# Kernel optimization log

Measured on AMD Instinct MI355X. Metric: run time of the kernel, lower is better.

Reference implementation:

```python
import jax, jax.numpy as jnp
import numpy as np
import math

B, QL, KL, H, QD, KD, VD = 4, 1024, 1024, 16, 1024, 1024, 1024
QH = QD // H  # 64
KH = KD // H  # 64


def setup_inputs() -> dict:
    rng = jax.random.key(0)
    ks = jax.random.split(rng, 8)
    return {
        "query": jax.random.normal(ks[0], (B, QL, QD), jnp.float32),
        "key": jax.random.normal(ks[1], (B, KL, KD), jnp.float32),
        "value": jax.random.normal(ks[2], (B, KL, VD), jnp.float32),
        "pad_mask": jax.random.randint(ks[3], (B, QL), 0, 2),
        "q_w": jax.random.uniform(ks[4], (H, QL, QH), jnp.float32),
        "k_w": jax.random.uniform(ks[5], (H, KL, KH), jnp.float32),
        "v_w": jax.random.uniform(ks[6], (H, KL, KH), jnp.float32),
        "o_w": jax.random.uniform(ks[7], (H * KH, QD), jnp.float32),
    }


def reference(query, key, value, pad_mask, q_w, k_w, v_w, o_w):
    b = query.shape[0]
    h, ql, qh = q_w.shape
    kl, kh = k_w.shape[1], k_w.shape[2]

    # mask construction: causal (triu, offset 1) OR pad mask tiled as in torch repeat+view
    causal = jnp.triu(jnp.ones((ql, kl), jnp.float32), 1) == 1            # [i, j]
    pad = jnp.tile(pad_mask, (1, kl)).reshape(b, ql, kl) == 1             # [b, i, j]
    mask = causal[None, :, :] | pad                                      # [b, i, j]

    # positional per-head projections: free index of input feature dim is summed out
    wq = jnp.einsum('biq,his->bhis', query, q_w)                          # [b, h, i, s]
    wk = jnp.einsum('bjk,hjt->bhjt', key, k_w)                            # [b, h, j, t]
    wv = jnp.einsum('bjv,hjt->bhjt', value, v_w)                          # [b, h, j, t]

    scale = math.sqrt(h)  # torch uses query.size()[1] == head_num after projection
    scores = jnp.einsum('bhis,bhjs->bhij', wq, wk) / scale                # [b, h, i, j]
    scores = jnp.where(mask[:, None, :, :], -jnp.inf, scores)
    scores = jnp.nan_to_num(scores)  # -inf -> finfo.min, matching torch.nan_to_num

    weight = jax.nn.softmax(scores, axis=0)  # unusual: softmax over the batch axis
    heads = jnp.einsum('bhij,bhjt->bhit', weight, wv)                     # [b, h, i, t]
    heads = heads.reshape(b, -1, h * kh)  # torch .view: reinterprets [h,i,t] as [i, h*t]
    return jnp.einsum('bit,to->bio', heads, o_w)                          # [b, i, q_dim]
```

## Files before the change

### kernel.cpp

```cpp
#include <hip/hip_runtime.h>
#include <hip/hip_bf16.h>

#define NB 4
#define NL 1024
#define NH 16
#define ND 1024
#define HD 64
#define FMIN_F32 (-3.4028234663852886e38f)
#define LOG2E 1.4426950408889634f

typedef __bf16 bf16x8 __attribute__((ext_vector_type(8)));
typedef float f32x4 __attribute__((ext_vector_type(4)));
typedef unsigned int u32;

static __device__ inline unsigned short f2bf(float f) {
    __hip_bfloat16 h = __float2bfloat16(f);
    return __builtin_bit_cast(unsigned short, h);
}

static __device__ inline void bfsplit(float x, unsigned short& hi, unsigned short& lo) {
    unsigned u = __builtin_bit_cast(unsigned, x);
    unsigned r = (u + 0x7FFFu + ((u >> 16) & 1u)) >> 16;
    hi = (unsigned short)r;
    float hf = __builtin_bit_cast(float, r << 16);
    lo = f2bf(x - hf);
}

static __device__ inline u32 pk2(unsigned short a, unsigned short b) {
    return (u32)a | ((u32)b << 16);
}

static __device__ __forceinline__ void gload16(void* lds, const void* g) {
    __builtin_amdgcn_global_load_lds(
        (const __attribute__((address_space(1))) u32*)g,
        (__attribute__((address_space(3))) u32*)lds, 16, 0, 0);
}

__global__ __launch_bounds__(256)
void rowsum_kernel(const float* __restrict__ q, const float* __restrict__ k,
                   const float* __restrict__ v, float* __restrict__ out) {
    int gw   = blockIdx.x * 4 + (threadIdx.x >> 6);
    int lane = threadIdx.x & 63;
    int tensor = gw >> 12;
    int row    = gw & 4095;
    const float* src = tensor == 0 ? q : (tensor == 1 ? k : v);
    const float* p = src + (size_t)row * ND;
    float s = 0.f;
#pragma unroll
    for (int t = 0; t < 4; ++t) {
        float4 x = *reinterpret_cast<const float4*>(p + t * 256 + lane * 4);
        s += (x.x + x.y) + (x.z + x.w);
    }
#pragma unroll
    for (int off = 32; off; off >>= 1) s += __shfl_xor(s, off);
    if (lane == 0) out[tensor * (NB * NL) + row] = s;
}

__global__ __launch_bounds__(256)
void prep_kernel(const float* __restrict__ k_w, const float* __restrict__ v_w,
                 const float* __restrict__ o_w, const float* __restrict__ sums,
                 unsigned short* __restrict__ kPhi, unsigned short* __restrict__ kPlo,
                 unsigned short* __restrict__ vP, unsigned short* __restrict__ BP,
                 float* __restrict__ S) {
    __shared__ float tile[64][132];
    __shared__ float vsL[256];
    const int tid = threadIdx.x;
    const int bx  = blockIdx.x;
    const float* vsum = sums + 2 * NB * NL;
    if (bx < 256) {
        const int h = bx >> 4, jt = bx & 15;
        char* hiT = (char*)kPhi + (size_t)(h * 16 + jt) * 8192;
        char* loT = (char*)kPlo + (size_t)(h * 16 + jt) * 8192;
        const int row = tid >> 2;
        const int s0  = (tid & 3) * 16;
        const float* src = k_w + ((size_t)(h * NL + jt * 64 + row)) * HD + s0;
#pragma unroll
        for (int t = 0; t < 4; ++t) {
            float4 x = reinterpret_cast<const float4*>(src)[t];
            unsigned short h0, h1, h2, h3, l0, l1, l2, l3;
            bfsplit(x.x, h0, l0); bfsplit(x.y, h1, l1);
            bfsplit(x.z, h2, l2); bfsplit(x.w, h3, l3);
            int off = (row * 128 + (s0 + 4 * t) * 2) ^ ((row & 7) << 4);
            *(uint2*)(hiT + off) = make_uint2(pk2(h0, h1), pk2(h2, h3));
            *(uint2*)(loT + off) = make_uint2(pk2(l0, l1), pk2(l2, l3));
        }
    } else if (bx < 512) {
        const int h = (bx - 256) >> 4, jt = (bx - 256) & 15;
#pragma unroll
        for (int t = 0; t < 4; ++t) {
            int id = tid + 256 * t;
            int j = id >> 4, t4 = (id & 15) * 4;
            *(float4*)&tile[j][t4] =
                *(const float4*)(v_w + ((size_t)(h * NL + jt * 64 + j)) * HD + t4);
        }
        vsL[tid] = vsum[(tid >> 6) * NL + jt * 64 + (tid & 63)];
        __syncthreads();
        char* vT_ = (char*)vP + (size_t)(h * 16 + jt) * 8192;
        const int trow = tid >> 2;
        const int jq   = (tid & 3) * 16;
#pragma unroll
        for (int q = 0; q < 4; ++q) {
            int j4 = jq + 4 * q;
            uint2 u;
            u.x = pk2(f2bf(tile[j4 + 0][trow]), f2bf(tile[j4 + 1][trow]));
            u.y = pk2(f2bf(tile[j4 + 2][trow]), f2bf(tile[j4 + 3][trow]));
            int off = (trow * 128 + j4 * 2) ^ ((trow & 7) << 4);
            *(uint2*)(vT_ + off) = u;
        }
        if (jt >= 1) {
            const int b = tid >> 6, t = tid & 63;
            float a = 0.f;
#pragma unroll 16
            for (int j = 0; j < 64; ++j)
                a = fmaf(vsL[b * 64 + j], tile[j][t], a);
            S[(((size_t)h * 16 + jt) * 4 + b) * 64 + t] = a;
        }
    } else {
        const int bxo = bx - 512;
        const int ot = bxo >> 4, kt = bxo & 15;
#pragma unroll
        for (int t = 0; t < 8; ++t) {
            int id = tid + 256 * t;
            int c = id >> 5, o4 = (id & 31) * 4;
            *(float4*)&tile[c][o4] =
                *(const float4*)(o_w + ((size_t)(kt * 64 + c)) * ND + ot * 128 + o4);
        }
        __syncthreads();
        char* bT = (char*)BP + (size_t)(ot * 16 + kt) * 16384;
#pragma unroll
        for (int t = 0; t < 8; ++t) {
            int id = tid + 256 * t;
            int ol = id >> 4, c4 = (id & 15) * 4;
            uint2 u;
            u.x = pk2(f2bf(tile[c4 + 0][ol]), f2bf(tile[c4 + 1][ol]));
            u.y = pk2(f2bf(tile[c4 + 2][ol]), f2bf(tile[c4 + 3][ol]));
            int off = (ol * 128 + c4 * 2) ^ ((ol & 7) << 4);
            *(uint2*)(bT + off) = u;
        }
    }
}

__global__ __launch_bounds__(512, 4)
void attn_kernel(const float* __restrict__ q_w, const int* __restrict__ pad,
                 const float* __restrict__ sums,
                 const unsigned short* __restrict__ kPhi,
                 const unsigned short* __restrict__ kPlo,
                 const unsigned short* __restrict__ vP,
                 const float* __restrict__ S,
                 unsigned short* __restrict__ AP) {
    __shared__ __align__(16) unsigned short kHi[2][4096], kLo[2][4096], vTl[2][4096];
    __shared__ __align__(16) unsigned short qHi[2048], qLo[2048];
    __shared__ __align__(16) unsigned short wlds[8192];
    __shared__ __align__(16) float qs4[128];
    __shared__ __align__(16) float ks4[2][256];
    __shared__ __align__(16) float vs4[2][256];
    __shared__ __align__(16) int   pm4[2][256];

    const float* qsum = sums;
    const float* ksum = sums + NB * NL;
    const float* vsum = sums + 2 * NB * NL;

    const int wid = blockIdx.x;
    const int gq  = wid >> 4;
    const int h   = wid & 15;
    const int itp = (gq < 16) ? (2 * gq) : (63 - 2 * gq);
    const int it0 = itp * 32;
    const int cut = (it0 >> 6) + 1;

    const int tid  = threadIdx.x;
    const int lane = tid & 63;
    const int w    = tid >> 6;
    const int l15  = lane & 15;
    const int kb   = (lane >> 4) * 16;

    {
        int row = tid >> 4;
        int s4  = (tid & 15) * 4;
        float4 x = *(const float4*)(q_w + ((size_t)(h * NL + it0 + row)) * HD + s4);
        unsigned short h0, h1, h2, h3, l0, l1, l2, l3;
        bfsplit(x.x, h0, l0); bfsplit(x.y, h1, l1);
        bfsplit(x.z, h2, l2); bfsplit(x.w, h3, l3);
        int off = (row * 128 + s4 * 2) ^ ((row & 7) << 4);
        *(uint2*)((char*)qHi + off) = make_uint2(pk2(h0, h1), pk2(h2, h3));
        *(uint2*)((char*)qLo + off) = make_uint2(pk2(l0, l1), pk2(l2, l3));
    }
    if (tid < 128) {
        int b = tid >> 5, i = tid & 31;
        qs4[i * 4 + b] = qsum[b * NL + it0 + i];
    }

    auto stage = [&](int buf, int jt) {
        const size_t tb = (size_t)(h * 16 + jt) * 8192 + tid * 16;
        gload16((char*)kHi[buf] + tid * 16, (const char*)kPhi + tb);
        gload16((char*)kLo[buf] + tid * 16, (const char*)kPlo + tb);
        gload16((char*)vTl[buf] + tid * 16, (const char*)vP + tb);
        if (tid < 256) {
            int b = tid >> 6, jj = tid & 63;
            ks4[buf][jj * 4 + b] = ksum[b * NL + jt * 64 + jj] * (LOG2E * 0.25f);
            vs4[buf][jj * 4 + b] = vsum[b * NL + jt * 64 + jj];
            pm4[buf][jj * 4 + b] = pad[b * NL + jt * 64 + jj];
        }
    };

    const int gmi = (w & 1) * 16;
    const int gnj = (w >> 1) * 16;
    const int pb  = w >> 1;
    const int pmh = (w & 1) * 16;

    f32x4 accP[4];
#pragma unroll
    for (int n = 0; n < 4; ++n) accP[n] = (f32x4){0.f, 0.f, 0.f, 0.f};

    stage(0, 0);
    __syncthreads();
    int cur = 0;

    const int i_sm  = gmi + l15;
    const int ig    = it0 + i_sm;
    const int jb_sm = gnj + (lane >> 4) * 4;
    const float4 qsv = *(const float4*)&qs4[i_sm * 4];
    const int woff = (i_sm * 128 + jb_sm * 2) ^ ((i_sm & 7) << 4);

    for (int jt = 0; jt < cut; ++jt) {
        const int j0 = jt * 64;
        if (jt + 1 < cut) stage(cur ^ 1, jt + 1);

        f32x4 gA = (f32x4){0.f, 0.f, 0.f, 0.f};
        f32x4 gB = (f32x4){0.f, 0.f, 0.f, 0.f};
#pragma unroll
        for (int ks = 0; ks < 2; ++ks) {
            const int arow = gnj + l15;
            const int brow = gmi + l15;
            const int aoff = (arow * 128 + ks * 64 + kb) ^ ((arow & 7) << 4);
            const int boff = (brow * 128 + ks * 64 + kb) ^ ((brow & 7) << 4);
            bf16x8 kHiF = __builtin_bit_cast(bf16x8, *(const uint4*)((const char*)kHi[cur] + aoff));
            bf16x8 kLoF = __builtin_bit_cast(bf16x8, *(const uint4*)((const char*)kLo[cur] + aoff));
            bf16x8 qHiF = __builtin_bit_cast(bf16x8, *(const uint4*)((const char*)qHi + boff));
            bf16x8 qLoF = __builtin_bit_cast(bf16x8, *(const uint4*)((const char*)qLo + boff));
            gA = __builtin_amdgcn_mfma_f32_16x16x32_bf16(kHiF, qHiF, gA, 0, 0, 0);
            gA = __builtin_amdgcn_mfma_f32_16x16x32_bf16(kLoF, qHiF, gA, 0, 0, 0);
            gB = __builtin_amdgcn_mfma_f32_16x16x32_bf16(kHiF, qLoF, gB, 0, 0, 0);
        }
        const f32x4 g = gA + gB;

        {
            float wv[4][4];
#pragma unroll
            for (int r = 0; r < 4; ++r) {
                const int j  = jb_sm + r;
                const int jg = j0 + j;
                const float4 ksv = *(const float4*)&ks4[cur][j * 4];
                const float4 vsv = *(const float4*)&vs4[cur][j * 4];
                const int4   pmv = *(const int4*)&pm4[cur][j * 4];
                const float gr = g[r];
                const bool causal = jg > ig;
                const float sb0 = (causal || pmv.x) ? FMIN_F32 : qsv.x * ksv.x * gr;
                const float sb1 = (causal || pmv.y) ? FMIN_F32 : qsv.y * ksv.y * gr;
                const float sb2 = (causal || pmv.z) ? FMIN_F32 : qsv.z * ksv.z * gr;
                const float sb3 = (causal || pmv.w) ? FMIN_F32 : qsv.w * ksv.w * gr;
                const float mx = fmaxf(fmaxf(sb0, sb1), fmaxf(sb2, sb3));
                const float e0 = __builtin_amdgcn_exp2f(sb0 - mx);
                const float e1 = __builtin_amdgcn_exp2f(sb1 - mx);
                const float e2 = __builtin_amdgcn_exp2f(sb2 - mx);
                const float e3 = __builtin_amdgcn_exp2f(sb3 - mx);
                const float inv = __builtin_amdgcn_rcpf((e0 + e1) + (e2 + e3));
                wv[r][0] = e0 * inv * vsv.x;
                wv[r][1] = e1 * inv * vsv.y;
                wv[r][2] = e2 * inv * vsv.z;
                wv[r][3] = e3 * inv * vsv.w;
            }
#pragma unroll
            for (int b = 0; b < 4; ++b) {
                uint2 p;
                p.x = pk2(f2bf(wv[0][b]), f2bf(wv[1][b]));
                p.y = pk2(f2bf(wv[2][b]), f2bf(wv[3][b]));
                *(uint2*)((char*)wlds + b * 4096 + woff) = p;
            }
        }
        asm volatile("s_waitcnt lgkmcnt(0)" ::: "memory");
        __builtin_amdgcn_s_barrier();
        __builtin_amdgcn_sched_barrier(0);

        __builtin_amdgcn_s_setprio(1);
#pragma unroll
        for (int ks = 0; ks < 2; ++ks) {
            const int arow = pmh + l15;
            const int aoff = pb * 4096 + ((arow * 128 + ks * 64 + kb) ^ ((arow & 7) << 4));
            bf16x8 aF = __builtin_bit_cast(bf16x8, *(const uint4*)((const char*)wlds + aoff));
#pragma unroll
            for (int n = 0; n < 4; ++n) {
                const int vrow = n * 16 + l15;
                const int voff = (vrow * 128 + ks * 64 + kb) ^ ((vrow & 7) << 4);
                bf16x8 bF = __builtin_bit_cast(bf16x8, *(const uint4*)((const char*)vTl[cur] + voff));
                accP[n] = __builtin_amdgcn_mfma_f32_16x16x32_bf16(aF, bF, accP[n], 0, 0, 0);
            }
        }
        __builtin_amdgcn_s_setprio(0);
        __syncthreads();
        cur ^= 1;
    }

    if (cut < 16) {
        float sv[4] = {0.f, 0.f, 0.f, 0.f};
        for (int jt = cut; jt < 16; ++jt) {
            const float* sp = S + (((size_t)h * 16 + jt) * 4 + pb) * 64;
#pragma unroll
            for (int n = 0; n < 4; ++n) sv[n] += sp[n * 16 + l15];
        }
#pragma unroll
        for (int n = 0; n < 4; ++n) {
            const float s4v = 0.25f * sv[n];
#pragma unroll
            for (int r = 0; r < 4; ++r) accP[n][r] += s4v;
        }
    }

    {
        const int ib = (it0 + pmh) >> 4;
        char* tbase = (char*)AP + (size_t)((pb * 16 + h) * 16) * 8192;
#pragma unroll
        for (int n = 0; n < 4; ++n)
#pragma unroll
            for (int r = 0; r < 4; ++r) {
                int kt = (lane >> 4) * 4 + r;
                int tt = n * 16 + l15;
                int off = (ib * 128 + tt * 2) ^ ((ib & 7) << 4);
                *(unsigned short*)(tbase + (size_t)kt * 8192 + off) = f2bf(accP[n][r]);
            }
    }
}

__global__ __launch_bounds__(256, 2)
void outgemm_kernel(const unsigned short* __restrict__ AP,
                    const unsigned short* __restrict__ BP,
                    float* __restrict__ out) {
    __shared__ __align__(16) unsigned short aL[3][4096];
    __shared__ __align__(16) unsigned short bL[3][8192];
    const int ox = blockIdx.x;
    const int my = blockIdx.y;
    const int tid  = threadIdx.x;
    const int lane = tid & 63;
    const int w    = tid >> 6;
    const int wr = (w & 1) * 32;
    const int wc = (w >> 1) * 64;
    const int l15  = lane & 15;
    const int kseg = (lane >> 4) * 16;

    f32x4 acc[2][4];
#pragma unroll
    for (int m = 0; m < 2; ++m)
#pragma unroll
        for (int n = 0; n < 4; ++n) acc[m][n] = (f32x4){0.f, 0.f, 0.f, 0.f};

    auto stage = [&](int buf, int kt) {
        const char* at = (const char*)AP + (size_t)(my * 16 + kt) * 8192;
        const char* bt = (const char*)BP + (size_t)(ox * 16 + kt) * 16384;
        gload16((char*)aL[buf] + tid * 16, at + tid * 16);
        gload16((char*)aL[buf] + 4096 + tid * 16, at + 4096 + tid * 16);
#pragma unroll
        for (int r = 0; r < 4; ++r)
            gload16((char*)bL[buf] + r * 4096 + tid * 16, bt + r * 4096 + tid * 16);
    };

    auto compute = [&](int cb) {
        __builtin_amdgcn_s_setprio(1);
#pragma unroll
        for (int ks = 0; ks < 2; ++ks) {
            bf16x8 aF[2], bF[4];
#pragma unroll
            for (int m = 0; m < 2; ++m) {
                int row = wr + m * 16 + l15;
                int off = (row * 128 + ks * 64 + kseg) ^ ((row & 7) << 4);
                aF[m] = __builtin_bit_cast(bf16x8, *(const uint4*)((const char*)aL[cb] + off));
            }
#pragma unroll
            for (int n = 0; n < 4; ++n) {
                int row = wc + n * 16 + l15;
                int off = (row * 128 + ks * 64 + kseg) ^ ((row & 7) << 4);
                bF[n] = __builtin_bit_cast(bf16x8, *(const uint4*)((const char*)bL[cb] + off));
            }
#pragma unroll
            for (int m = 0; m < 2; ++m)
#pragma unroll
                for (int n = 0; n < 4; ++n)
                    acc[m][n] = __builtin_amdgcn_mfma_f32_16x16x32_bf16(
                        aF[m], bF[n], acc[m][n], 0, 0, 0);
        }
        __builtin_amdgcn_s_setprio(0);
    };

    stage(0, 0);
    stage(1, 1);
    for (int kt = 0; kt < 15; ++kt) {
        asm volatile("s_waitcnt vmcnt(6)" ::: "memory");
        __builtin_amdgcn_s_barrier();
        __builtin_amdgcn_sched_barrier(0);
        if (kt + 2 < 16) stage((kt + 2) % 3, kt + 2);
        compute(kt % 3);
    }
    asm volatile("s_waitcnt vmcnt(0)" ::: "memory");
    __builtin_amdgcn_s_barrier();
    __builtin_amdgcn_sched_barrier(0);
    compute(15 % 3);

#pragma unroll
    for (int m = 0; m < 2; ++m)
#pragma unroll
        for (int n = 0; n < 4; ++n)
#pragma unroll
            for (int r = 0; r < 4; ++r) {
                int row = my * 64 + wr + m * 16 + (lane >> 4) * 4 + r;
                int col = ox * 128 + wc + n * 16 + l15;
                out[(size_t)row * ND + col] = acc[m][n][r];
            }
}

extern "C" void kernel_launch(void* const* d_in, const int* in_sizes, int n_in,
                              void* d_out, int out_size, void* d_ws, size_t ws_size,
                              hipStream_t stream) {
    const float* query = (const float*)d_in[0];
    const float* key   = (const float*)d_in[1];
    const float* value = (const float*)d_in[2];
    const int*   pad   = (const int*)d_in[3];
    const float* q_w   = (const float*)d_in[4];
    const float* k_w   = (const float*)d_in[5];
    const float* v_w   = (const float*)d_in[6];
    const float* o_w   = (const float*)d_in[7];
    float* out = (float*)d_out;

    char* W = (char*)d_ws;
    float*          sums = (float*)W;
    unsigned short* kPhi = (unsigned short*)(W + 49152);
    unsigned short* kPlo = (unsigned short*)(W + 2146304);
    unsigned short* vP   = (unsigned short*)(W + 4243456);
    unsigned short* BP   = (unsigned short*)(W + 6340608);
    unsigned short* AP   = (unsigned short*)(W + 8437760);

    float* S = out;

    rowsum_kernel<<<3 * (NB * NL) / 4, 256, 0, stream>>>(query, key, value, sums);

    prep_kernel<<<640, 256, 0, stream>>>(k_w, v_w, o_w, sums, kPhi, kPlo, vP, BP, S);

    attn_kernel<<<512, 512, 0, stream>>>(q_w, pad, sums, kPhi, kPlo, vP, S, AP);

    dim3 gg(8, 64);
    outgemm_kernel<<<gg, 256, 0, stream>>>(AP, BP, out);
}
```

Measured before the change: 69.95 us.

## Precompute masked key/value sums in prep kernel and use packed bf16 conversion

Moves the per-key sum scaling, the pad-mask lookup and the batch interleaving out of the attention kernel's staging loop into extra blocks of the prep kernel. The results are written as interleaved float arrays (scaled key sums, value sums, additive mask bias) into scratch space inside the output buffer, so attention staging becomes three vectorised float4 loads. The score computation turns into an fma plus bias, with a select for the causal case. Scalar bf16 conversion and packing are replaced by the packed v_cvt_pk_bf16_f32 instruction throughout. The trade-off is an extra global round trip for the precomputed arrays and reliance on the output buffer as scratch before the final GEMM overwrites it.

```diff
diff --git a/kernel.cpp b/kernel.cpp
--- a/kernel.cpp
+++ b/kernel.cpp
@@ -18,16 +18,17 @@
     return __builtin_bit_cast(unsigned short, h);
 }
 
-static __device__ inline void bfsplit(float x, unsigned short& hi, unsigned short& lo) {
-    unsigned u = __builtin_bit_cast(unsigned, x);
-    unsigned r = (u + 0x7FFFu + ((u >> 16) & 1u)) >> 16;
-    hi = (unsigned short)r;
-    float hf = __builtin_bit_cast(float, r << 16);
-    lo = f2bf(x - hf);
-}
-
-static __device__ inline u32 pk2(unsigned short a, unsigned short b) {
-    return (u32)a | ((u32)b << 16);
+static __device__ __forceinline__ u32 cvtpk(float a, float b) {
+    u32 r;
+    asm("v_cvt_pk_bf16_f32 %0, %1, %2" : "=v"(r) : "v"(a), "v"(b));
+    return r;
+}
+
+static __device__ __forceinline__ void bfsplit2(float x, float y, u32& hiPk, u32& loPk) {
+    hiPk = cvtpk(x, y);
+    float hx = __builtin_bit_cast(float, hiPk << 16);
+    float hy = __builtin_bit_cast(float, hiPk & 0xffff0000u);
+    loPk = cvtpk(x - hx, y - hy);
 }
 
 static __device__ __forceinline__ void gload16(void* lds, const void* g) {
@@ -59,13 +60,16 @@
 __global__ __launch_bounds__(256)
 void prep_kernel(const float* __restrict__ k_w, const float* __restrict__ v_w,
                  const float* __restrict__ o_w, const float* __restrict__ sums,
+                 const int* __restrict__ pad,
                  unsigned short* __restrict__ kPhi, unsigned short* __restrict__ kPlo,
                  unsigned short* __restrict__ vP, unsigned short* __restrict__ BP,
-                 float* __restrict__ S) {
+                 float* __restrict__ S, float* __restrict__ ksm,
+                 float* __restrict__ vsm, float* __restrict__ bsm) {
     __shared__ float tile[64][132];
     __shared__ float vsL[256];
     const int tid = threadIdx.x;
     const int bx  = blockIdx.x;
+    const float* ksum = sums + NB * NL;
     const float* vsum = sums + 2 * NB * NL;
     if (bx < 256) {
         const int h = bx >> 4, jt = bx & 15;
@@ -77,12 +81,12 @@
 #pragma unroll
         for (int t = 0; t < 4; ++t) {
             float4 x = reinterpret_cast<const float4*>(src)[t];
-            unsigned short h0, h1, h2, h3, l0, l1, l2, l3;
-            bfsplit(x.x, h0, l0); bfsplit(x.y, h1, l1);
-            bfsplit(x.z, h2, l2); bfsplit(x.w, h3, l3);
+            u32 h01, l01, h23, l23;
+            bfsplit2(x.x, x.y, h01, l01);
+            bfsplit2(x.z, x.w, h23, l23);
             int off = (row * 128 + (s0 + 4 * t) * 2) ^ ((row & 7) << 4);
-            *(uint2*)(hiT + off) = make_uint2(pk2(h0, h1), pk2(h2, h3));
-            *(uint2*)(loT + off) = make_uint2(pk2(l0, l1), pk2(l2, l3));
+            *(uint2*)(hiT + off) = make_uint2(h01, h23);
+            *(uint2*)(loT + off) = make_uint2(l01, l23);
         }
     } else if (bx < 512) {
         const int h = (bx - 256) >> 4, jt = (bx - 256) & 15;
@@ -102,8 +106,8 @@
         for (int q = 0; q < 4; ++q) {
             int j4 = jq + 4 * q;
             uint2 u;
-            u.x = pk2(f2bf(tile[j4 + 0][trow]), f2bf(tile[j4 + 1][trow]));
-            u.y = pk2(f2bf(tile[j4 + 2][trow]), f2bf(tile[j4 + 3][trow]));
+            u.x = cvtpk(tile[j4 + 0][trow], tile[j4 + 1][trow]);
+            u.y = cvtpk(tile[j4 + 2][trow], tile[j4 + 3][trow]);
             int off = (trow * 128 + j4 * 2) ^ ((trow & 7) << 4);
             *(uint2*)(vT_ + off) = u;
         }
@@ -115,7 +119,7 @@
                 a = fmaf(vsL[b * 64 + j], tile[j][t], a);
             S[(((size_t)h * 16 + jt) * 4 + b) * 64 + t] = a;
         }
-    } else {
+    } else if (bx < 640) {
         const int bxo = bx - 512;
         const int ot = bxo >> 4, kt = bxo & 15;
 #pragma unroll
@@ -132,21 +136,28 @@
             int id = tid + 256 * t;
             int ol = id >> 4, c4 = (id & 15) * 4;
             uint2 u;
-            u.x = pk2(f2bf(tile[c4 + 0][ol]), f2bf(tile[c4 + 1][ol]));
-            u.y = pk2(f2bf(tile[c4 + 2][ol]), f2bf(tile[c4 + 3][ol]));
+            u.x = cvtpk(tile[c4 + 0][ol], tile[c4 + 1][ol]);
+            u.y = cvtpk(tile[c4 + 2][ol], tile[c4 + 3][ol]);
             int off = (ol * 128 + c4 * 2) ^ ((ol & 7) << 4);
             *(uint2*)(bT + off) = u;
         }
+    } else {
+        const int e = (bx - 640) * 256 + tid;
+        const int j = e >> 2, b = e & 3;
+        const int pm = pad[b * NL + j];
+        ksm[e] = pm ? 0.f : ksum[b * NL + j] * (LOG2E * 0.25f);
+        vsm[e] = vsum[b * NL + j];
+        bsm[e] = pm ? FMIN_F32 : 0.f;
     }
 }
 
 __global__ __launch_bounds__(512, 4)
-void attn_kernel(const float* __restrict__ q_w, const int* __restrict__ pad,
-                 const float* __restrict__ sums,
+void attn_kernel(const float* __restrict__ q_w, const float* __restrict__ sums,
                  const unsigned short* __restrict__ kPhi,
                  const unsigned short* __restrict__ kPlo,
                  const unsigned short* __restrict__ vP,
-                 const float* __restrict__ S,
+                 const float* __restrict__ ksm, const float* __restrict__ vsm,
+                 const float* __restrict__ bsm, const float* __restrict__ S,
                  unsigned short* __restrict__ AP) {
     __shared__ __align__(16) unsigned short kHi[2][4096], kLo[2][4096], vTl[2][4096];
     __shared__ __align__(16) unsigned short qHi[2048], qLo[2048];
@@ -154,11 +165,9 @@
     __shared__ __align__(16) float qs4[128];
     __shared__ __align__(16) float ks4[2][256];
     __shared__ __align__(16) float vs4[2][256];
-    __shared__ __align__(16) int   pm4[2][256];
+    __shared__ __align__(16) float bs4[2][256];
 
     const float* qsum = sums;
-    const float* ksum = sums + NB * NL;
-    const float* vsum = sums + 2 * NB * NL;
 
     const int wid = blockIdx.x;
     const int gq  = wid >> 4;
@@ -177,12 +186,12 @@
         int row = tid >> 4;
         int s4  = (tid & 15) * 4;
         float4 x = *(const float4*)(q_w + ((size_t)(h * NL + it0 + row)) * HD + s4);
-        unsigned short h0, h1, h2, h3, l0, l1, l2, l3;
-        bfsplit(x.x, h0, l0); bfsplit(x.y, h1, l1);
-        bfsplit(x.z, h2, l2); bfsplit(x.w, h3, l3);
+        u32 h01, l01, h23, l23;
+        bfsplit2(x.x, x.y, h01, l01);
+        bfsplit2(x.z, x.w, h23, l23);
         int off = (row * 128 + s4 * 2) ^ ((row & 7) << 4);
-        *(uint2*)((char*)qHi + off) = make_uint2(pk2(h0, h1), pk2(h2, h3));
-        *(uint2*)((char*)qLo + off) = make_uint2(pk2(l0, l1), pk2(l2, l3));
+        *(uint2*)((char*)qHi + off) = make_uint2(h01, h23);
+        *(uint2*)((char*)qLo + off) = make_uint2(l01, l23);
     }
     if (tid < 128) {
         int b = tid >> 5, i = tid & 31;
@@ -190,16 +199,19 @@
     }
 
     auto stage = [&](int buf, int jt) {
+        float4 tv;
+        float* tdst = nullptr;
+        if (tid < 192) {
+            int seg = tid >> 6, l = tid & 63;
+            const float* src = seg == 0 ? ksm : (seg == 1 ? vsm : bsm);
+            tv = *(const float4*)(src + jt * 256 + l * 4);
+            tdst = (seg == 0 ? ks4[buf] : (seg == 1 ? vs4[buf] : bs4[buf])) + l * 4;
+        }
         const size_t tb = (size_t)(h * 16 + jt) * 8192 + tid * 16;
         gload16((char*)kHi[buf] + tid * 16, (const char*)kPhi + tb);
         gload16((char*)kLo[buf] + tid * 16, (const char*)kPlo + tb);
         gload16((char*)vTl[buf] + tid * 16, (const char*)vP + tb);
-        if (tid < 256) {
-            int b = tid >> 6, jj = tid & 63;
-            ks4[buf][jj * 4 + b] = ksum[b * NL + jt * 64 + jj] * (LOG2E * 0.25f);
-            vs4[buf][jj * 4 + b] = vsum[b * NL + jt * 64 + jj];
-            pm4[buf][jj * 4 + b] = pad[b * NL + jt * 64 + jj];
-        }
+        if (tid < 192) *(float4*)tdst = tv;
     };
 
     const int gmi = (w & 1) * 16;
@@ -251,13 +263,17 @@
                 const int jg = j0 + j;
                 const float4 ksv = *(const float4*)&ks4[cur][j * 4];
                 const float4 vsv = *(const float4*)&vs4[cur][j * 4];
-                const int4   pmv = *(const int4*)&pm4[cur][j * 4];
+                const float4 bsv = *(const float4*)&bs4[cur][j * 4];
                 const float gr = g[r];
                 const bool causal = jg > ig;
-                const float sb0 = (causal || pmv.x) ? FMIN_F32 : qsv.x * ksv.x * gr;
-                const float sb1 = (causal || pmv.y) ? FMIN_F32 : qsv.y * ksv.y * gr;
-                const float sb2 = (causal || pmv.z) ? FMIN_F32 : qsv.z * ksv.z * gr;
-                const float sb3 = (causal || pmv.w) ? FMIN_F32 : qsv.w * ksv.w * gr;
+                float sb0 = fmaf(qsv.x * ksv.x, gr, bsv.x);
+                float sb1 = fmaf(qsv.y * ksv.y, gr, bsv.y);
+                float sb2 = fmaf(qsv.z * ksv.z, gr, bsv.z);
+                float sb3 = fmaf(qsv.w * ksv.w, gr, bsv.w);
+                sb0 = causal ? 0.f : sb0;
+                sb1 = causal ? 0.f : sb1;
+                sb2 = causal ? 0.f : sb2;
+                sb3 = causal ? 0.f : sb3;
                 const float mx = fmaxf(fmaxf(sb0, sb1), fmaxf(sb2, sb3));
                 const float e0 = __builtin_amdgcn_exp2f(sb0 - mx);
                 const float e1 = __builtin_amdgcn_exp2f(sb1 - mx);
@@ -272,8 +288,8 @@
 #pragma unroll
             for (int b = 0; b < 4; ++b) {
                 uint2 p;
-                p.x = pk2(f2bf(wv[0][b]), f2bf(wv[1][b]));
-                p.y = pk2(f2bf(wv[2][b]), f2bf(wv[3][b]));
+                p.x = cvtpk(wv[0][b], wv[1][b]);
+                p.y = cvtpk(wv[2][b], wv[3][b]);
                 *(uint2*)((char*)wlds + b * 4096 + woff) = p;
             }
         }
@@ -436,13 +452,18 @@
     unsigned short* BP   = (unsigned short*)(W + 6340608);
     unsigned short* AP   = (unsigned short*)(W + 8437760);
 
-    float* S = out;
+    float* S   = out;
+    float* ksm = out + 65536;
+    float* vsm = out + 69632;
+    float* bsm = out + 73728;
 
     rowsum_kernel<<<3 * (NB * NL) / 4, 256, 0, stream>>>(query, key, value, sums);
 
-    prep_kernel<<<640, 256, 0, stream>>>(k_w, v_w, o_w, sums, kPhi, kPlo, vP, BP, S);
-
-    attn_kernel<<<512, 512, 0, stream>>>(q_w, pad, sums, kPhi, kPlo, vP, S, AP);
+    prep_kernel<<<656, 256, 0, stream>>>(k_w, v_w, o_w, sums, pad,
+                                         kPhi, kPlo, vP, BP, S, ksm, vsm, bsm);
+
+    attn_kernel<<<512, 512, 0, stream>>>(q_w, sums, kPhi, kPlo, vP,
+                                         ksm, vsm, bsm, S, AP);
 
     dim3 gg(8, 64);
     outgemm_kernel<<<gg, 256, 0, stream>>>(AP, BP, out);
```

After: 79.34 us. 1.13x slower.
